# Performance work log

Hardware: AMD Instinct MI355X
Metric: run time of the kernel (lower is better)

Reference implementation:

```python
import jax, jax.numpy as jnp
import numpy as np

B, S, D = 2, 2048, 1024
H, DK, DV = 16, 64, 64

def setup_inputs() -> dict:
    key = jax.random.key(0)
    ks = jax.random.split(key, 5)
    scale = 1.0 / np.sqrt(D)  # xavier-ish
    return {
        "Q": jax.random.normal(ks[0], (B, S, D), dtype=jnp.float32),
        "attn_mask": jax.random.uniform(ks[1], (B, S), dtype=jnp.float32),
        "W_Q": jax.random.normal(ks[2], (H * DK, D), dtype=jnp.float32) * scale,
        "b_Q": jnp.zeros((H * DK,), dtype=jnp.float32),
        "W_K": jax.random.normal(ks[3], (H * DK, D), dtype=jnp.float32) * scale,
        "b_K": jnp.zeros((H * DK,), dtype=jnp.float32),
        "W_V": jax.random.normal(ks[4], (H * DV, D), dtype=jnp.float32) * scale,
        "b_V": jnp.zeros((H * DV,), dtype=jnp.float32),
    }

def reference(Q, attn_mask, W_Q, b_Q, W_K, b_K, W_V, b_V):
    b, s, _ = Q.shape
    # projections -> [B, H, S, d]
    q = (Q @ W_Q.T + b_Q).reshape(b, s, H, DK).transpose(0, 2, 1, 3)
    k = (Q @ W_K.T + b_K).reshape(b, s, H, DK).transpose(0, 2, 1, 3)
    v = (Q @ W_V.T + b_V).reshape(b, s, H, DV).transpose(0, 2, 1, 3)
    # exp-based attention (NOT stable softmax), multiplicative mask
    scores = jnp.einsum('bhqd,bhkd->bhqk', q, k) / np.sqrt(DK)
    scores = jnp.exp(scores)
    # mask [B, S_key] broadcast over heads and queries -> [B, 1, 1, S]
    scores = scores * attn_mask[:, None, None, :]
    attn = scores / (jnp.sum(scores, axis=-1, keepdims=True) + 1e-8)
    context = jnp.einsum('bhqk,bhkd->bhqd', attn, v)
    # [B, H, S, DV] -> [B, S, H*DV]
    return context.transpose(0, 2, 1, 3).reshape(b, s, H * DV)
```

## Files before the change

### kernel.cpp

```cpp
#include <hip/hip_runtime.h>
#include <hip/hip_bf16.h>
#include <math.h>

#define BATCH  2
#define S_LEN  2048
#define DMODEL 1024
#define NH     16
#define DHEAD  64

typedef __attribute__((ext_vector_type(8))) short bf16x8;
typedef __attribute__((ext_vector_type(4))) float f32x4;

#define MFMA16(a,b,c) __builtin_amdgcn_mfma_f32_16x16x32_bf16((a),(b),(c),0,0,0)

#define QSCALE 0.18033688011110793f
#define EXP2F(x) __builtin_amdgcn_exp2f(x)

__device__ __forceinline__ unsigned int pkbf(float a, float b) {
    __hip_bfloat162 h = __float22bfloat162_rn(make_float2(a, b));
    union { __hip_bfloat162 h; unsigned int u; } v; v.h = h; return v.u;
}

__global__ __launch_bounds__(256) void cvt_all(
    const float* __restrict__ Q,  const float* __restrict__ WQ,
    const float* __restrict__ WK, const float* __restrict__ WV,
    const float* __restrict__ msk,
    unsigned short* __restrict__ Qbf, unsigned short* __restrict__ Wbf,
    unsigned short* __restrict__ mbf)
{
    int i = blockIdx.x * blockDim.x + threadIdx.x;
    const float* src;
    unsigned short* dst;
    int off;
    if (i < 524288) {
        src = Q; dst = Qbf; off = i;
    } else if (i < 917504) {
        int j = i - 524288;
        int which = j >> 17;
        src = (which == 0) ? WQ : ((which == 1) ? WK : WV);
        dst = Wbf + ((size_t)which << 20);
        off = j & 131071;
    } else {
        int j = i - 917504;
        if (j >= 512) return;
        src = msk; dst = mbf; off = j;
    }
    float4 a = ((const float4*)src)[2*off];
    float4 b = ((const float4*)src)[2*off + 1];
    uint4 o;
    o.x = pkbf(a.x, a.y); o.y = pkbf(a.z, a.w);
    o.z = pkbf(b.x, b.y); o.w = pkbf(b.z, b.w);
    ((uint4*)dst)[off] = o;
}

__global__ __launch_bounds__(256) void proj_mfma(
    const unsigned short* __restrict__ Abf,
    const unsigned short* __restrict__ Wbf,
    const float* __restrict__ bQ, const float* __restrict__ bK,
    const float* __restrict__ bV, const float* __restrict__ mask,
    unsigned short* __restrict__ qw, unsigned short* __restrict__ kw,
    unsigned short* __restrict__ vt)
{
    __shared__ union {
        struct { unsigned short A[2][4096]; unsigned short B[2][4096]; } s;
        unsigned short Ct[128*132];
    } sm;

    const int tid  = threadIdx.x;
    const int lane = tid & 63;
    const int wv   = tid >> 6;
    const int wm   = (wv >> 1) * 64;
    const int wn   = (wv & 1) * 64;
    const int q15  = lane & 15;
    const int quad = lane >> 4;
    const int z    = blockIdx.z;
    const int n0   = blockIdx.x * 128;
    const int m0   = blockIdx.y * 128;

    const unsigned short* Wz = Wbf + (size_t)z * DMODEL * DMODEL;
    const float* bias = (z == 0) ? bQ : ((z == 1) ? bK : bV);

    const int r0 = tid >> 2,          c0 = (tid & 3) * 8;
    const int r1 = (tid + 256) >> 2,  c1 = c0;

    f32x4 zero4 = {0.f, 0.f, 0.f, 0.f};
    f32x4 acc[4][4];
    #pragma unroll
    for (int i = 0; i < 4; ++i)
        #pragma unroll
        for (int j = 0; j < 4; ++j) acc[i][j] = zero4;

    uint4 a0, a1, b0, b1;
    a0 = *(const uint4*)(Abf + (size_t)(m0 + r0) * DMODEL + c0);
    a1 = *(const uint4*)(Abf + (size_t)(m0 + r1) * DMODEL + c1);
    b0 = *(const uint4*)(Wz  + (size_t)(n0 + r0) * DMODEL + c0);
    b1 = *(const uint4*)(Wz  + (size_t)(n0 + r1) * DMODEL + c1);

    for (int t = 0; t < 32; ++t) {
        const int buf = t & 1;
        *(uint4*)(sm.s.A[buf] + r0*32 + c0) = a0;
        *(uint4*)(sm.s.A[buf] + r1*32 + c1) = a1;
        *(uint4*)(sm.s.B[buf] + r0*32 + c0) = b0;
        *(uint4*)(sm.s.B[buf] + r1*32 + c1) = b1;
        const int kn = (t < 31) ? (t + 1) * 32 : 0;
        a0 = *(const uint4*)(Abf + (size_t)(m0 + r0) * DMODEL + kn + c0);
        a1 = *(const uint4*)(Abf + (size_t)(m0 + r1) * DMODEL + kn + c1);
        b0 = *(const uint4*)(Wz  + (size_t)(n0 + r0) * DMODEL + kn + c0);
        b1 = *(const uint4*)(Wz  + (size_t)(n0 + r1) * DMODEL + kn + c1);
        __syncthreads();

        bf16x8 af[4], bf[4];
        #pragma unroll
        for (int i = 0; i < 4; ++i)
            af[i] = *(const bf16x8*)(sm.s.A[buf] + (wm + i*16 + q15) * 32 + quad * 8);
        #pragma unroll
        for (int j = 0; j < 4; ++j)
            bf[j] = *(const bf16x8*)(sm.s.B[buf] + (wn + j*16 + q15) * 32 + quad * 8);

        if (z < 2) {
            #pragma unroll
            for (int i = 0; i < 4; ++i)
                #pragma unroll
                for (int j = 0; j < 4; ++j)
                    acc[i][j] = MFMA16(bf[j], af[i], acc[i][j]);
        } else {
            #pragma unroll
            for (int i = 0; i < 4; ++i)
                #pragma unroll
                for (int j = 0; j < 4; ++j)
                    acc[i][j] = MFMA16(af[i], bf[j], acc[i][j]);
        }
    }

    __syncthreads();

    if (z < 2) {
        const float qs = (z == 0) ? QSCALE : 1.0f;
        #pragma unroll
        for (int i = 0; i < 4; ++i) {
            int ml = wm + i*16 + q15;
            #pragma unroll
            for (int j = 0; j < 4; ++j) {
                int nl = wn + j*16 + quad*4;
                float4 b4 = *(const float4*)(bias + n0 + nl);
                f32x4 v = acc[i][j];
                uint2 u;
                u.x = pkbf((v.x + b4.x)*qs, (v.y + b4.y)*qs);
                u.y = pkbf((v.z + b4.z)*qs, (v.w + b4.w)*qs);
                *(uint2*)&sm.Ct[ml*132 + nl] = u;
            }
        }
    } else {
        #pragma unroll
        for (int i = 0; i < 4; ++i) {
            int ml = wm + i*16 + quad*4;
            int sg = m0 + ml;
            int b2 = sg >> 11, s0g = sg & 2047;
            float4 mk4 = *(const float4*)(mask + (size_t)b2*S_LEN + s0g);
            #pragma unroll
            for (int j = 0; j < 4; ++j) {
                int nl = wn + j*16 + q15;
                float bv = bias[n0 + nl];
                f32x4 v = acc[i][j];
                uint2 u;
                u.x = pkbf((v.x + bv)*mk4.x, (v.y + bv)*mk4.y);
                u.y = pkbf((v.z + bv)*mk4.z, (v.w + bv)*mk4.w);
                *(uint2*)&sm.Ct[nl*132 + ml] = u;
            }
        }
    }
    __syncthreads();

    {
        int row  = tid >> 1;
        int half = (tid & 1) * 64;
        const uint4* src = (const uint4*)&sm.Ct[row*132 + half];
        unsigned short* dst;
        if (z < 2) {
            unsigned short* outp = (z == 0) ? qw : kw;
            int mg = m0 + row;  int b2 = mg >> 11, s = mg & 2047;
            int n  = n0 + half; int hh = n >> 6;
            dst = outp + (((size_t)b2*NH + hh)*S_LEN + s)*DHEAD;
        } else {
            int n  = n0 + row;  int hh = n >> 6, dv = n & 63;
            int b2 = m0 >> 11, s0 = m0 & 2047;
            dst = vt + (((size_t)b2*NH + hh)*DHEAD + dv)*S_LEN + s0 + half;
        }
        #pragma unroll
        for (int c = 0; c < 8; ++c) ((uint4*)dst)[c] = src[c];
    }
}

__global__ __launch_bounds__(512, 4) void attn_mfma(
    const unsigned short* __restrict__ qw, const unsigned short* __restrict__ kw,
    const unsigned short* __restrict__ vt, const unsigned short* __restrict__ mbf,
    float* __restrict__ out)
{
    __shared__ __align__(16) unsigned short Ks[2][64][72];
    __shared__ __align__(16) unsigned short Vs[2][64][72];
    __shared__ __align__(16) unsigned short Ms[2][72];

    const int tid  = threadIdx.x;
    const int lane = tid & 63;
    const int wv   = tid >> 6;
    const int q15  = lane & 15;
    const int quad = lane >> 4;
    const int q0   = blockIdx.x * 128;
    const int h    = blockIdx.y;
    const int b    = blockIdx.z;

    const size_t headoff = ((size_t)b * NH + h) * S_LEN * DHEAD;
    const unsigned short* qb = qw + headoff;
    const unsigned short* kb = kw + headoff;
    const unsigned short* vb = vt + headoff;
    const unsigned short* mb = mbf + (size_t)b * S_LEN;

    const unsigned short* qr = qb + (size_t)(q0 + wv*16 + q15)*DHEAD;
    bf16x8 qf0 = *(const bf16x8*)(qr + quad*8);
    bf16x8 qf1 = *(const bf16x8*)(qr + 32 + quad*8);

    const int srow = tid >> 3;
    const int scol = (tid & 7) * 8;
    const int prow = (srow & 32) + ((srow >> 2) & 1) * 16
                   + ((srow >> 3) & 3) * 4 + (srow & 3);

    f32x4 zero4 = {0.f, 0.f, 0.f, 0.f};
    f32x4 oacc[4];
    f32x4 dacc = zero4;
    #pragma unroll
    for (int nj = 0; nj < 4; ++nj) oacc[nj] = zero4;

    uint4 kr, vr, mr = {0,0,0,0};
    kr = *(const uint4*)(kb + (size_t)srow*DHEAD + scol);
    vr = *(const uint4*)(vb + (size_t)srow*S_LEN + scol);
    if (tid < 8) mr = *(const uint4*)(mb + tid*8);

    for (int t = 0; t < 32; ++t) {
        const int buf = t & 1;
        const int k0  = t * 64;
        *(uint4*)&Ks[buf][prow][scol] = kr;
        *(uint4*)&Vs[buf][srow][scol] = vr;
        if (tid < 8) *(uint4*)&Ms[buf][tid*8] = mr;
        const int kn = (t < 31) ? k0 + 64 : 0;
        kr = *(const uint4*)(kb + (size_t)(kn + srow)*DHEAD + scol);
        vr = *(const uint4*)(vb + (size_t)srow*S_LEN + kn + scol);
        if (tid < 8) mr = *(const uint4*)(mb + kn + tid*8);
        __syncthreads();

        f32x4 s[4];
        #pragma unroll
        for (int ks = 0; ks < 4; ++ks) {
            bf16x8 kf0 = *(const bf16x8*)&Ks[buf][ks*16 + q15][quad*8];
            bf16x8 kf1 = *(const bf16x8*)&Ks[buf][ks*16 + q15][32 + quad*8];
            f32x4 a = MFMA16(kf0, qf0, zero4);
            s[ks] = MFMA16(kf1, qf1, a);
        }
        uint4 u0, u1;
        u0.x = pkbf(EXP2F(s[0][0]), EXP2F(s[0][1]));
        u0.y = pkbf(EXP2F(s[0][2]), EXP2F(s[0][3]));
        u0.z = pkbf(EXP2F(s[1][0]), EXP2F(s[1][1]));
        u0.w = pkbf(EXP2F(s[1][2]), EXP2F(s[1][3]));
        u1.x = pkbf(EXP2F(s[2][0]), EXP2F(s[2][1]));
        u1.y = pkbf(EXP2F(s[2][2]), EXP2F(s[2][3]));
        u1.z = pkbf(EXP2F(s[3][0]), EXP2F(s[3][1]));
        u1.w = pkbf(EXP2F(s[3][2]), EXP2F(s[3][3]));
        union { uint4 u; bf16x8 h; } c0, c1;
        c0.u = u0; c1.u = u1;
        bf16x8 pf0 = c0.h;
        bf16x8 pf1 = c1.h;
        bf16x8 mf0 = *(const bf16x8*)&Ms[buf][quad*8];
        bf16x8 mf1 = *(const bf16x8*)&Ms[buf][32 + quad*8];
        dacc = MFMA16(pf0, mf0, dacc);
        dacc = MFMA16(pf1, mf1, dacc);
        #pragma unroll
        for (int nj = 0; nj < 4; ++nj) {
            bf16x8 vf0 = *(const bf16x8*)&Vs[buf][nj*16 + q15][quad*8];
            bf16x8 vf1 = *(const bf16x8*)&Vs[buf][nj*16 + q15][32 + quad*8];
            oacc[nj] = MFMA16(pf0, vf0, oacc[nj]);
            oacc[nj] = MFMA16(pf1, vf1, oacc[nj]);
        }
    }

    #pragma unroll
    for (int r = 0; r < 4; ++r) {
        float inv = 1.0f / (dacc[r] + 1e-8f);
        size_t row = ((size_t)b*S_LEN + q0 + wv*16 + quad*4 + r)*DMODEL + h*DHEAD;
        #pragma unroll
        for (int nj = 0; nj < 4; ++nj)
            out[row + nj*16 + q15] = oacc[nj][r] * inv;
    }
}

extern "C" void kernel_launch(void* const* d_in, const int* in_sizes, int n_in,
                              void* d_out, int out_size, void* d_ws, size_t ws_size,
                              hipStream_t stream) {
    const float* Q    = (const float*)d_in[0];
    const float* msk  = (const float*)d_in[1];
    const float* W_Q  = (const float*)d_in[2];
    const float* b_Q  = (const float*)d_in[3];
    const float* W_K  = (const float*)d_in[4];
    const float* b_K  = (const float*)d_in[5];
    const float* W_V  = (const float*)d_in[6];
    const float* b_V  = (const float*)d_in[7];
    float* out = (float*)d_out;

    unsigned short* wsu = (unsigned short*)d_ws;
    unsigned short* Qbf = wsu;
    unsigned short* Wbf = Qbf + (size_t)4096*1024;
    unsigned short* qwb = Wbf + (size_t)3*1024*1024;
    unsigned short* kwb = qwb + (size_t)4*1024*1024;
    unsigned short* vtb = kwb + (size_t)4*1024*1024;
    unsigned short* mbf = vtb + (size_t)4*1024*1024;

    cvt_all<<<3586, 256, 0, stream>>>(Q, W_Q, W_K, W_V, msk, Qbf, Wbf, mbf);

    proj_mfma<<<dim3(8, 32, 3), 256, 0, stream>>>(
        Qbf, Wbf, b_Q, b_K, b_V, msk, qwb, kwb, vtb);

    attn_mfma<<<dim3(S_LEN/128, NH, BATCH), 512, 0, stream>>>(
        qwb, kwb, vtb, mbf, out);
}
```

Measured before the change: 190.4 us.

## Use direct global-to-LDS loads in projection GEMM and halve attention query tile

New measurement: 189.9 us. Within noise of the previous version (-0.3%).

```diff
diff --git a/kernel.cpp b/kernel.cpp
--- a/kernel.cpp
+++ b/kernel.cpp
@@ -19,6 +19,11 @@
 __device__ __forceinline__ unsigned int pkbf(float a, float b) {
     __hip_bfloat162 h = __float22bfloat162_rn(make_float2(a, b));
     union { __hip_bfloat162 h; unsigned int u; } v; v.h = h; return v.u;
+}
+__device__ __forceinline__ void gl2lds16(const void* g, void* l) {
+    __builtin_amdgcn_global_load_lds(
+        (const __attribute__((address_space(1))) void*)(g),
+        (__attribute__((address_space(3))) void*)(l), 16, 0, 0);
 }
 
 __global__ __launch_bounds__(256) void cvt_all(
@@ -80,8 +85,10 @@
     const unsigned short* Wz = Wbf + (size_t)z * DMODEL * DMODEL;
     const float* bias = (z == 0) ? bQ : ((z == 1) ? bK : bV);
 
-    const int r0 = tid >> 2,          c0 = (tid & 3) * 8;
-    const int r1 = (tid + 256) >> 2,  c1 = c0;
+    const int o0 = tid * 16;
+    const int r0 = o0 >> 6,  cc0 = (o0 & 63) >> 1;
+    const int o1 = o0 + 4096;
+    const int r1 = o1 >> 6,  cc1 = (o1 & 63) >> 1;
 
     f32x4 zero4 = {0.f, 0.f, 0.f, 0.f};
     f32x4 acc[4][4];
@@ -90,24 +97,21 @@
         #pragma unroll
         for (int j = 0; j < 4; ++j) acc[i][j] = zero4;
 
-    uint4 a0, a1, b0, b1;
-    a0 = *(const uint4*)(Abf + (size_t)(m0 + r0) * DMODEL + c0);
-    a1 = *(const uint4*)(Abf + (size_t)(m0 + r1) * DMODEL + c1);
-    b0 = *(const uint4*)(Wz  + (size_t)(n0 + r0) * DMODEL + c0);
-    b1 = *(const uint4*)(Wz  + (size_t)(n0 + r1) * DMODEL + c1);
+    gl2lds16(Abf + (size_t)(m0 + r0)*DMODEL + cc0, (char*)sm.s.A[0] + o0);
+    gl2lds16(Abf + (size_t)(m0 + r1)*DMODEL + cc1, (char*)sm.s.A[0] + o1);
+    gl2lds16(Wz  + (size_t)(n0 + r0)*DMODEL + cc0, (char*)sm.s.B[0] + o0);
+    gl2lds16(Wz  + (size_t)(n0 + r1)*DMODEL + cc1, (char*)sm.s.B[0] + o1);
 
     for (int t = 0; t < 32; ++t) {
         const int buf = t & 1;
-        *(uint4*)(sm.s.A[buf] + r0*32 + c0) = a0;
-        *(uint4*)(sm.s.A[buf] + r1*32 + c1) = a1;
-        *(uint4*)(sm.s.B[buf] + r0*32 + c0) = b0;
-        *(uint4*)(sm.s.B[buf] + r1*32 + c1) = b1;
-        const int kn = (t < 31) ? (t + 1) * 32 : 0;
-        a0 = *(const uint4*)(Abf + (size_t)(m0 + r0) * DMODEL + kn + c0);
-        a1 = *(const uint4*)(Abf + (size_t)(m0 + r1) * DMODEL + kn + c1);
-        b0 = *(const uint4*)(Wz  + (size_t)(n0 + r0) * DMODEL + kn + c0);
-        b1 = *(const uint4*)(Wz  + (size_t)(n0 + r1) * DMODEL + kn + c1);
         __syncthreads();
+        if (t < 31) {
+            const int kn = (t + 1) * 32;
+            gl2lds16(Abf + (size_t)(m0 + r0)*DMODEL + kn + cc0, (char*)sm.s.A[buf^1] + o0);
+            gl2lds16(Abf + (size_t)(m0 + r1)*DMODEL + kn + cc1, (char*)sm.s.A[buf^1] + o1);
+            gl2lds16(Wz  + (size_t)(n0 + r0)*DMODEL + kn + cc0, (char*)sm.s.B[buf^1] + o0);
+            gl2lds16(Wz  + (size_t)(n0 + r1)*DMODEL + kn + cc1, (char*)sm.s.B[buf^1] + o1);
+        }
 
         bf16x8 af[4], bf[4];
         #pragma unroll
@@ -191,7 +195,7 @@
     }
 }
 
-__global__ __launch_bounds__(512, 4) void attn_mfma(
+__global__ __launch_bounds__(256, 4) void attn_mfma(
     const unsigned short* __restrict__ qw, const unsigned short* __restrict__ kw,
     const unsigned short* __restrict__ vt, const unsigned short* __restrict__ mbf,
     float* __restrict__ out)
@@ -205,7 +209,7 @@
     const int wv   = tid >> 6;
     const int q15  = lane & 15;
     const int quad = lane >> 4;
-    const int q0   = blockIdx.x * 128;
+    const int q0   = blockIdx.x * 64;
     const int h    = blockIdx.y;
     const int b    = blockIdx.z;
 
@@ -221,8 +225,7 @@
 
     const int srow = tid >> 3;
     const int scol = (tid & 7) * 8;
-    const int prow = (srow & 32) + ((srow >> 2) & 1) * 16
-                   + ((srow >> 3) & 3) * 4 + (srow & 3);
+    const int prow = ((srow >> 2) & 1) * 16 + ((srow >> 3) & 3) * 4 + (srow & 3);
 
     f32x4 zero4 = {0.f, 0.f, 0.f, 0.f};
     f32x4 oacc[4];
@@ -230,20 +233,26 @@
     #pragma unroll
     for (int nj = 0; nj < 4; ++nj) oacc[nj] = zero4;
 
-    uint4 kr, vr, mr = {0,0,0,0};
-    kr = *(const uint4*)(kb + (size_t)srow*DHEAD + scol);
-    vr = *(const uint4*)(vb + (size_t)srow*S_LEN + scol);
+    uint4 kr0, kr1, vr0, vr1, mr = {0,0,0,0};
+    kr0 = *(const uint4*)(kb + (size_t)(srow)     *DHEAD + scol);
+    kr1 = *(const uint4*)(kb + (size_t)(srow + 32)*DHEAD + scol);
+    vr0 = *(const uint4*)(vb + (size_t)(srow)     *S_LEN + scol);
+    vr1 = *(const uint4*)(vb + (size_t)(srow + 32)*S_LEN + scol);
     if (tid < 8) mr = *(const uint4*)(mb + tid*8);
 
     for (int t = 0; t < 32; ++t) {
         const int buf = t & 1;
         const int k0  = t * 64;
-        *(uint4*)&Ks[buf][prow][scol] = kr;
-        *(uint4*)&Vs[buf][srow][scol] = vr;
+        *(uint4*)&Ks[buf][prow][scol]      = kr0;
+        *(uint4*)&Ks[buf][prow + 32][scol] = kr1;
+        *(uint4*)&Vs[buf][srow][scol]      = vr0;
+        *(uint4*)&Vs[buf][srow + 32][scol] = vr1;
         if (tid < 8) *(uint4*)&Ms[buf][tid*8] = mr;
         const int kn = (t < 31) ? k0 + 64 : 0;
-        kr = *(const uint4*)(kb + (size_t)(kn + srow)*DHEAD + scol);
-        vr = *(const uint4*)(vb + (size_t)srow*S_LEN + kn + scol);
+        kr0 = *(const uint4*)(kb + (size_t)(kn + srow)     *DHEAD + scol);
+        kr1 = *(const uint4*)(kb + (size_t)(kn + srow + 32)*DHEAD + scol);
+        vr0 = *(const uint4*)(vb + (size_t)(srow)     *S_LEN + kn + scol);
+        vr1 = *(const uint4*)(vb + (size_t)(srow + 32)*S_LEN + kn + scol);
         if (tid < 8) mr = *(const uint4*)(mb + kn + tid*8);
         __syncthreads();
 
@@ -317,6 +326,6 @@
     proj_mfma<<<dim3(8, 32, 3), 256, 0, stream>>>(
         Qbf, Wbf, b_Q, b_K, b_V, msk, qwb, kwb, vtb);
 
-    attn_mfma<<<dim3(S_LEN/128, NH, BATCH), 512, 0, stream>>>(
+    attn_mfma<<<dim3(S_LEN/64, NH, BATCH), 256, 0, stream>>>(
         qwb, kwb, vtb, mbf, out);
 }
```
